# Kernel tuning notes

Hardware: AMD Instinct MI355X
Metric: run time of the kernel (lower is better)

Reference implementation:

```python
import jax, jax.numpy as jnp
import numpy as np

B, S, D = 2, 4096, 1024
H, DK = 16, 64          # heads, QK feature dim per head
DV = D // H             # output features per head = 64
QKV_OUT = (2 * DK + DV) * H  # 3072


def setup_inputs() -> dict:
    key = jax.random.key(0)
    k1, k2, k3, k4, k5 = jax.random.split(key, 5)
    x = jax.random.normal(k1, (B, S, D), dtype=jnp.float32)
    Wqkv = jax.random.normal(k2, (D, QKV_OUT), dtype=jnp.float32) * (1.0 / np.sqrt(D))
    bqkv = jnp.zeros((QKV_OUT,), dtype=jnp.float32)
    Wproj = jax.random.normal(k3, (D, D), dtype=jnp.float32) * (1.0 / np.sqrt(D))
    bproj = jnp.zeros((D,), dtype=jnp.float32)
    return {"x": x, "Wqkv": Wqkv, "bqkv": bqkv, "Wproj": Wproj, "bproj": bproj}


def reference(x, Wqkv, bqkv, Wproj, bproj):
    # QKV projection: [B,S,(2*DK+DV)*H]
    qkv = x @ Wqkv + bqkv
    q_len = DK * H
    Q = qkv[:, :, :q_len].reshape(B, S, H, DK).transpose(0, 2, 1, 3)        # [B,H,S,DK]
    K = qkv[:, :, q_len:2 * q_len].reshape(B, S, H, DK).transpose(0, 2, 1, 3)
    V = qkv[:, :, 2 * q_len:].reshape(B, S, H, DV).transpose(0, 2, 1, 3)    # [B,H,S,DV]

    scores = jnp.einsum("bhqd,bhkd->bhqk", Q, K) * (1.0 / np.sqrt(DK))
    # Faithful to source: causal mask is tril(ones) with zeros -> -inf,
    # i.e. +1.0 is ADDED on allowed positions (harmless constant shift per row).
    tril = jnp.tril(jnp.ones((S, S), dtype=jnp.float32))
    mask = jnp.where(tril == 0, -jnp.inf, tril)
    scores = scores + mask
    attn = jax.nn.softmax(scores, axis=-1)  # dropout disabled (p=0 / eval)

    out = jnp.einsum("bhqk,bhkd->bhqd", attn, V)            # [B,H,S,DV]
    out = out.transpose(0, 2, 1, 3).reshape(B, S, H * DV)   # [B,S,D]
    return out @ Wproj + bproj
```

## Files before the change

kernel.cpp:

```cpp
#include <hip/hip_runtime.h>
#include <stdint.h>


typedef __bf16 bf16x8 __attribute__((ext_vector_type(8)));
typedef float f32x4 __attribute__((ext_vector_type(4)));
typedef unsigned short u16x8 __attribute__((ext_vector_type(8)));
typedef unsigned short u16x4 __attribute__((ext_vector_type(4)));
typedef unsigned int u32x4 __attribute__((ext_vector_type(4)));

__device__ __forceinline__ unsigned short f2bf(float f) {
  unsigned u = __builtin_bit_cast(unsigned, f);
  u += 0x7FFFu + ((u >> 16) & 1u);
  return (unsigned short)(u >> 16);
}

__device__ __forceinline__ float fast_exp2(float x) {
#if __has_builtin(__builtin_amdgcn_exp2f)
  return __builtin_amdgcn_exp2f(x);
#else
  return exp2f(x);
#endif
}

__device__ __forceinline__ void gload16(const void* g, void* l) {
  __builtin_amdgcn_global_load_lds(
      (__attribute__((address_space(1))) unsigned int*)(uintptr_t)g,
      (__attribute__((address_space(3))) unsigned int*)(unsigned int)(uintptr_t)l,
      16, 0, 0);
}

__global__ void k_cvt_bf16(const float* __restrict__ in,
                           unsigned short* __restrict__ out, int n8) {
  int i = blockIdx.x * blockDim.x + threadIdx.x;
  if (i >= n8) return;
  const float4* p = reinterpret_cast<const float4*>(in) + (size_t)i * 2;
  float4 a = p[0], b = p[1];
  u16x8 o;
  o[0] = f2bf(a.x); o[1] = f2bf(a.y); o[2] = f2bf(a.z); o[3] = f2bf(a.w);
  o[4] = f2bf(b.x); o[5] = f2bf(b.y); o[6] = f2bf(b.z); o[7] = f2bf(b.w);
  *(reinterpret_cast<u16x8*>(out) + i) = o;
}

__global__ void k_transcvt(const float* __restrict__ in,
                           unsigned short* __restrict__ out, int K, int N) {
  __shared__ float tile[32][33];
  int tk0 = blockIdx.y << 5, tn0 = blockIdx.x << 5;
  int t = threadIdx.x;
  int r = t >> 3, c4 = (t & 7) << 2;
  float4 v = *reinterpret_cast<const float4*>(&in[(size_t)(tk0 + r) * N + tn0 + c4]);
  tile[r][c4 + 0] = v.x; tile[r][c4 + 1] = v.y;
  tile[r][c4 + 2] = v.z; tile[r][c4 + 3] = v.w;
  __syncthreads();
  u16x4 o;
  o[0] = f2bf(tile[c4 + 0][r]); o[1] = f2bf(tile[c4 + 1][r]);
  o[2] = f2bf(tile[c4 + 2][r]); o[3] = f2bf(tile[c4 + 3][r]);
  *reinterpret_cast<u16x4*>(&out[(size_t)(tn0 + r) * K + tk0 + c4]) = o;
}

__device__ __forceinline__ void gemm_core_db(
    const unsigned short* __restrict__ A, const unsigned short* __restrict__ Bt,
    unsigned short (*Al)[128 * 32], unsigned short (*Bl)[128 * 32],
    int m0, int n0, f32x4 acc[4][4]) {
  const int t = threadIdx.x;
  const int lane = t & 63;
  const int w = t >> 6;
  const int wr = w >> 1, wc = w & 1;
  const int l15 = lane & 15, l4 = lane >> 4;

  const int c0 = t, c1 = t + 256;
  const int r0 = c0 >> 2, s0 = ((c0 & 3) << 3) ^ (((r0 >> 1) & 3) << 3);
  const int r1 = c1 >> 2, s1 = ((c1 & 3) << 3) ^ (((r1 >> 1) & 3) << 3);
  const size_t ga0 = (size_t)(m0 + r0) * 1024 + s0;
  const size_t ga1 = (size_t)(m0 + r1) * 1024 + s1;
  const size_t gb0 = (size_t)(n0 + r0) * 1024 + s0;
  const size_t gb1 = (size_t)(n0 + r1) * 1024 + s1;

  int aidx[4], bidx[4];
#pragma unroll
  for (int m = 0; m < 4; ++m) {
    int row = wr * 64 + m * 16 + l15;
    aidx[m] = row * 32 + ((l4 * 8) ^ (((row >> 1) & 3) << 3));
    row = wc * 64 + m * 16 + l15;
    bidx[m] = row * 32 + ((l4 * 8) ^ (((row >> 1) & 3) << 3));
  }

#define GSTAGE(bufi, kofs)                                   \
  do {                                                       \
    gload16(A + ga0 + (kofs), Al[bufi] + c0 * 8);            \
    gload16(A + ga1 + (kofs), Al[bufi] + c1 * 8);            \
    gload16(Bt + gb0 + (kofs), Bl[bufi] + c0 * 8);           \
    gload16(Bt + gb1 + (kofs), Bl[bufi] + c1 * 8);           \
  } while (0)

  GSTAGE(0, 0);
  asm volatile("s_waitcnt vmcnt(0)" ::: "memory");
  __builtin_amdgcn_s_barrier();

#pragma unroll 1
  for (int it = 0; it < 32; ++it) {
    const int cur = it & 1;
    if (it + 1 < 32) GSTAGE(cur ^ 1, (it + 1) * 32);
    bf16x8 af[4], bfr[4];
#pragma unroll
    for (int m = 0; m < 4; ++m)
      af[m] = *reinterpret_cast<const bf16x8*>(Al[cur] + aidx[m]);
#pragma unroll
    for (int n = 0; n < 4; ++n)
      bfr[n] = *reinterpret_cast<const bf16x8*>(Bl[cur] + bidx[n]);
    __builtin_amdgcn_s_setprio(1);
#pragma unroll
    for (int m = 0; m < 4; ++m)
#pragma unroll
      for (int n = 0; n < 4; ++n)
        acc[m][n] = __builtin_amdgcn_mfma_f32_16x16x32_bf16(af[m], bfr[n],
                                                            acc[m][n], 0, 0, 0);
    __builtin_amdgcn_s_setprio(0);
    asm volatile("s_waitcnt vmcnt(0)" ::: "memory");
    __builtin_amdgcn_s_barrier();
  }
#undef GSTAGE
}

__global__ __launch_bounds__(256) void k_gemm_qkv(
    const unsigned short* __restrict__ A, const unsigned short* __restrict__ Bt,
    const float* __restrict__ bias, unsigned short* __restrict__ Qb,
    unsigned short* __restrict__ Kb, unsigned short* __restrict__ VTb) {
  __shared__ unsigned short Al[2][128 * 32];
  __shared__ unsigned short Bl[2][128 * 32];
  const int lane = threadIdx.x & 63, w = threadIdx.x >> 6;
  const int wr = w >> 1, wc = w & 1;
  const int l15 = lane & 15, l4 = lane >> 4;
  const int m0 = blockIdx.y << 7, n0 = blockIdx.x << 7;
  const float C1 = 0.18033688011112043f;

  f32x4 acc[4][4] = {};
  gemm_core_db(A, Bt, Al, Bl, m0, n0, acc);

#pragma unroll
  for (int m = 0; m < 4; ++m) {
#pragma unroll
    for (int n = 0; n < 4; ++n) {
#pragma unroll
      for (int j = 0; j < 4; ++j) {
        int row = m0 + wr * 64 + m * 16 + l4 * 4 + j;
        int col = n0 + wc * 64 + n * 16 + l15;
        float v = acc[m][n][j] + bias[col];
        int b = row >> 12, s = row & 4095;
        if (col < 1024) {
          int hh = col >> 6, d = col & 63;
          Qb[((size_t)(b * 16 + hh) * 4096 + s) * 64 + d] = f2bf(v * C1);
        } else if (col < 2048) {
          int cc = col - 1024; int hh = cc >> 6, d = cc & 63;
          Kb[((size_t)(b * 16 + hh) * 4096 + s) * 64 + d] = f2bf(v);
        } else {
          int cc = col - 2048; int hh = cc >> 6, d = cc & 63;
          VTb[((size_t)(b * 16 + hh) * 64 + d) * 4096 + s] = f2bf(v);
        }
      }
    }
  }
}

__global__ __launch_bounds__(256) void k_gemm_proj(
    const unsigned short* __restrict__ A, const unsigned short* __restrict__ Bt,
    const float* __restrict__ bias, float* __restrict__ out) {
  __shared__ unsigned short Al[2][128 * 32];
  __shared__ unsigned short Bl[2][128 * 32];
  const int lane = threadIdx.x & 63, w = threadIdx.x >> 6;
  const int wr = w >> 1, wc = w & 1;
  const int l15 = lane & 15, l4 = lane >> 4;
  const int m0 = blockIdx.y << 7, n0 = blockIdx.x << 7;

  f32x4 acc[4][4] = {};
  gemm_core_db(A, Bt, Al, Bl, m0, n0, acc);

#pragma unroll
  for (int m = 0; m < 4; ++m) {
#pragma unroll
    for (int n = 0; n < 4; ++n) {
#pragma unroll
      for (int j = 0; j < 4; ++j) {
        int row = m0 + wr * 64 + m * 16 + l4 * 4 + j;
        int col = n0 + wc * 64 + n * 16 + l15;
        out[(size_t)row * 1024 + col] = acc[m][n][j] + bias[col];
      }
    }
  }
}

__global__ __launch_bounds__(256, 4) void k_attn(
    const unsigned short* __restrict__ Qb, const unsigned short* __restrict__ Kb,
    const unsigned short* __restrict__ VTb, unsigned short* __restrict__ Ob) {
  __shared__ unsigned short Kl[2][64 * 64];
  __shared__ unsigned short Vl[2][64 * 64];
  const int t = threadIdx.x;
  const int lane = t & 63, w = t >> 6;
  const int l15 = lane & 15, l4 = lane >> 4;
  const int idx = blockIdx.x;
  const int qt = 31 - (idx >> 5);
  const int bh = idx & 31;
  const size_t qkbase = (size_t)bh * 4096 * 64;
  const size_t vbase = (size_t)bh * 64 * 4096;
  const int b = bh >> 4, hh = bh & 15;
  const int wrow0 = qt * 128 + w * 32;
  const int nt = 2 * qt + 2;

  const int c0 = t, c1 = t + 256;
  const int kr0 = c0 >> 3, ks0 = ((c0 & 7) << 3) ^ ((kr0 & 7) << 3);
  const int kr1 = c1 >> 3, ks1 = ((c1 & 7) << 3) ^ ((kr1 & 7) << 3);

#define STAGE(bufi, jt)                                                             \
  do {                                                                              \
    gload16(Kb + qkbase + (size_t)((jt) * 64 + kr0) * 64 + ks0, &Kl[bufi][c0 * 8]); \
    gload16(Kb + qkbase + (size_t)((jt) * 64 + kr1) * 64 + ks1, &Kl[bufi][c1 * 8]); \
    gload16(VTb + vbase + (size_t)kr0 * 4096 + (jt) * 64 + ks0, &Vl[bufi][c0 * 8]); \
    gload16(VTb + vbase + (size_t)kr1 * 4096 + (jt) * 64 + ks1, &Vl[bufi][c1 * 8]); \
  } while (0)

  bf16x8 qf[2][2];
#pragma unroll
  for (int m = 0; m < 2; ++m)
#pragma unroll
    for (int kk = 0; kk < 2; ++kk)
      qf[m][kk] = *reinterpret_cast<const bf16x8*>(
          &Qb[qkbase + (size_t)(wrow0 + m * 16 + l15) * 64 + kk * 32 + l4 * 8]);

  f32x4 oacc[2][4] = {};
  float lsum[2] = {};

  STAGE(0, 0);
  asm volatile("s_waitcnt vmcnt(0)" ::: "memory");
  __builtin_amdgcn_s_barrier();

  for (int j = 0; j < nt; ++j) {
    const int cur = j & 1;
    if (j + 1 < nt) STAGE(cur ^ 1, j + 1);

    const int jk0 = j * 64;
    const bool active = (jk0 <= wrow0 + 31);
    const bool needmask = active && (jk0 + 63 > wrow0);

    if (active) {
#pragma unroll
      for (int h = 0; h < 2; ++h) {
        f32x4 sch[2][2] = {};
        __builtin_amdgcn_s_setprio(1);
#pragma unroll
        for (int nn = 0; nn < 2; ++nn) {
          int krow = (h * 2 + nn) * 16 + l15;
#pragma unroll
          for (int kk = 0; kk < 2; ++kk) {
            int kcol = (kk * 32 + l4 * 8) ^ ((krow & 7) << 3);
            bf16x8 kfr = *reinterpret_cast<const bf16x8*>(&Kl[cur][krow * 64 + kcol]);
#pragma unroll
            for (int m = 0; m < 2; ++m)
              sch[m][nn] = __builtin_amdgcn_mfma_f32_16x16x32_bf16(
                  kfr, qf[m][kk], sch[m][nn], 0, 0, 0);
          }
        }
        __builtin_amdgcn_s_setprio(0);

        bf16x8 pa[2];
#pragma unroll
        for (int m = 0; m < 2; ++m) {
#pragma unroll
          for (int nn = 0; nn < 2; ++nn)
#pragma unroll
            for (int r = 0; r < 4; ++r)
              sch[m][nn][r] = fast_exp2(sch[m][nn][r]);
          if (needmask) {
            const int qg = wrow0 + m * 16 + l15;
#pragma unroll
            for (int nn = 0; nn < 2; ++nn) {
              const int kb = jk0 + (h * 2 + nn) * 16 + l4 * 4;
#pragma unroll
              for (int r = 0; r < 4; ++r)
                if (kb + r > qg) sch[m][nn][r] = 0.f;
            }
          }
#pragma unroll
          for (int nn = 0; nn < 2; ++nn)
#pragma unroll
            for (int r = 0; r < 4; ++r)
              lsum[m] += sch[m][nn][r];

          unsigned A0, A1, B0, B1;
          asm("v_cvt_pk_bf16_f32 %0, %1, %2"
              : "=v"(A0) : "v"(sch[m][0][0]), "v"(sch[m][0][1]));
          asm("v_cvt_pk_bf16_f32 %0, %1, %2"
              : "=v"(A1) : "v"(sch[m][0][2]), "v"(sch[m][0][3]));
          asm("v_cvt_pk_bf16_f32 %0, %1, %2"
              : "=v"(B0) : "v"(sch[m][1][0]), "v"(sch[m][1][1]));
          asm("v_cvt_pk_bf16_f32 %0, %1, %2"
              : "=v"(B1) : "v"(sch[m][1][2]), "v"(sch[m][1][3]));
          asm("v_permlane32_swap_b32 %0, %1" : "+v"(A0), "+v"(B0));
          asm("v_permlane16_swap_b32 %0, %1" : "+v"(A0), "+v"(B0));
          asm("v_permlane32_swap_b32 %0, %1" : "+v"(A1), "+v"(B1));
          asm("v_permlane16_swap_b32 %0, %1" : "+v"(A1), "+v"(B1));
          u32x4 pw;
          pw[0] = A0; pw[1] = A1; pw[2] = B0; pw[3] = B1;
          pa[m] = __builtin_bit_cast(bf16x8, pw);
        }

        __builtin_amdgcn_s_setprio(1);
#pragma unroll
        for (int nn2 = 0; nn2 < 4; ++nn2) {
          int vr = nn2 * 16 + l15;
          int vc = (h * 32 + l4 * 8) ^ ((vr & 7) << 3);
          bf16x8 vf = *reinterpret_cast<const bf16x8*>(&Vl[cur][vr * 64 + vc]);
          oacc[0][nn2] = __builtin_amdgcn_mfma_f32_16x16x32_bf16(
              pa[0], vf, oacc[0][nn2], 0, 0, 0);
          oacc[1][nn2] = __builtin_amdgcn_mfma_f32_16x16x32_bf16(
              pa[1], vf, oacc[1][nn2], 0, 0, 0);
        }
        __builtin_amdgcn_s_setprio(0);
      }
    }

    asm volatile("s_waitcnt vmcnt(0)" ::: "memory");
    __builtin_amdgcn_s_barrier();
  }
#undef STAGE

#pragma unroll
  for (int m = 0; m < 2; ++m) {
    lsum[m] += __shfl_xor(lsum[m], 16);
    lsum[m] += __shfl_xor(lsum[m], 32);
  }
#pragma unroll
  for (int m = 0; m < 2; ++m)
#pragma unroll
    for (int jj = 0; jj < 4; ++jj) {
      float inv = 1.0f / __shfl(lsum[m], l4 * 4 + jj);
      int srow = wrow0 + m * 16 + l4 * 4 + jj;
#pragma unroll
      for (int nn = 0; nn < 4; ++nn) {
        int col = hh * 64 + nn * 16 + l15;
        Ob[((size_t)(b * 4096 + srow)) * 1024 + col] =
            __builtin_bit_cast(unsigned short, (__bf16)(oacc[m][nn][jj] * inv));
      }
    }
}

extern "C" void kernel_launch(void* const* d_in, const int* in_sizes, int n_in,
                              void* d_out, int out_size, void* d_ws, size_t ws_size,
                              hipStream_t stream) {
  const float* x = (const float*)d_in[0];
  const float* Wqkv = (const float*)d_in[1];
  const float* bqkv = (const float*)d_in[2];
  const float* Wproj = (const float*)d_in[3];
  const float* bproj = (const float*)d_in[4];

  char* ws = (char*)d_ws;
  unsigned short* xb  = (unsigned short*)(ws);
  unsigned short* Wqb = (unsigned short*)(ws + 16777216);
  unsigned short* Wpb = (unsigned short*)(ws + 23068672);
  unsigned short* Qb  = (unsigned short*)(ws + 25165824);
  unsigned short* Kb  = (unsigned short*)(ws + 41943040);
  unsigned short* VTb = (unsigned short*)(ws + 58720256);
  unsigned short* Ob  = (unsigned short*)(ws + 75497472);

  k_cvt_bf16<<<dim3(8388608 / 8 / 256), dim3(256), 0, stream>>>(x, xb, 8388608 / 8);
  k_transcvt<<<dim3(3072 / 32, 1024 / 32), dim3(256), 0, stream>>>(Wqkv, Wqb, 1024, 3072);
  k_transcvt<<<dim3(1024 / 32, 1024 / 32), dim3(256), 0, stream>>>(Wproj, Wpb, 1024, 1024);
  k_gemm_qkv<<<dim3(3072 / 128, 8192 / 128), dim3(256), 0, stream>>>(xb, Wqb, bqkv, Qb, Kb, VTb);
  k_attn<<<dim3(1024), dim3(256), 0, stream>>>(Qb, Kb, VTb, Ob);
  k_gemm_proj<<<dim3(1024 / 128, 8192 / 128), dim3(256), 0, stream>>>(Ob, Wpb, bproj, (float*)d_out);
}
```

Baseline: 220.4 us.

## Load GEMM B operand straight from global into registers, unroll double buffer

The shared GEMM core now stages only the A tile through LDS. The B fragments are read directly from global memory into registers, double-buffered across a two-step unrolled loop, which removes the B LDS writes and reads and halves LDS use. The QKV epilogue hoists the bias loads, splits the Q/K and V paths by block column, and writes V-transpose as packed 4-element stores. Occupancy hints of 3 blocks are added. In exchange, global B loads are less coalesced and each wave reloads B from L2, and register pressure rises.

```diff
diff --git a/kernel.cpp b/kernel.cpp
--- a/kernel.cpp
+++ b/kernel.cpp
@@ -57,10 +57,9 @@
   *reinterpret_cast<u16x4*>(&out[(size_t)(tn0 + r) * K + tk0 + c4]) = o;
 }
 
-__device__ __forceinline__ void gemm_core_db(
+__device__ __forceinline__ void gemm_core_bg(
     const unsigned short* __restrict__ A, const unsigned short* __restrict__ Bt,
-    unsigned short (*Al)[128 * 32], unsigned short (*Bl)[128 * 32],
-    int m0, int n0, f32x4 acc[4][4]) {
+    unsigned short (*Al)[128 * 32], int m0, int n0, f32x4 acc[4][4]) {
   const int t = threadIdx.x;
   const int lane = t & 63;
   const int w = t >> 6;
@@ -72,61 +71,73 @@
   const int r1 = c1 >> 2, s1 = ((c1 & 3) << 3) ^ (((r1 >> 1) & 3) << 3);
   const size_t ga0 = (size_t)(m0 + r0) * 1024 + s0;
   const size_t ga1 = (size_t)(m0 + r1) * 1024 + s1;
-  const size_t gb0 = (size_t)(n0 + r0) * 1024 + s0;
-  const size_t gb1 = (size_t)(n0 + r1) * 1024 + s1;
-
-  int aidx[4], bidx[4];
+
+  int aidx[4];
 #pragma unroll
   for (int m = 0; m < 4; ++m) {
     int row = wr * 64 + m * 16 + l15;
     aidx[m] = row * 32 + ((l4 * 8) ^ (((row >> 1) & 3) << 3));
-    row = wc * 64 + m * 16 + l15;
-    bidx[m] = row * 32 + ((l4 * 8) ^ (((row >> 1) & 3) << 3));
-  }
-
-#define GSTAGE(bufi, kofs)                                   \
+  }
+
+  const unsigned short* bp[4];
+#pragma unroll
+  for (int n = 0; n < 4; ++n)
+    bp[n] = Bt + (size_t)(n0 + wc * 64 + n * 16 + l15) * 1024 + l4 * 8;
+
+#define ASTAGE(bufi, kofs)                                   \
   do {                                                       \
     gload16(A + ga0 + (kofs), Al[bufi] + c0 * 8);            \
     gload16(A + ga1 + (kofs), Al[bufi] + c1 * 8);            \
-    gload16(Bt + gb0 + (kofs), Bl[bufi] + c0 * 8);           \
-    gload16(Bt + gb1 + (kofs), Bl[bufi] + c1 * 8);           \
   } while (0)
 
-  GSTAGE(0, 0);
+#define BLOAD(dst, kofs)                                                     \
+  do {                                                                       \
+    _Pragma("unroll") for (int n = 0; n < 4; ++n)                            \
+      dst[n] = *reinterpret_cast<const bf16x8*>(bp[n] + (kofs));             \
+  } while (0)
+
+#define BODY(bufi, breg)                                                     \
+  do {                                                                       \
+    bf16x8 af[4];                                                            \
+    _Pragma("unroll") for (int m = 0; m < 4; ++m)                            \
+      af[m] = *reinterpret_cast<const bf16x8*>(Al[bufi] + aidx[m]);          \
+    __builtin_amdgcn_s_setprio(1);                                           \
+    _Pragma("unroll") for (int m = 0; m < 4; ++m)                            \
+      _Pragma("unroll") for (int n = 0; n < 4; ++n)                          \
+        acc[m][n] = __builtin_amdgcn_mfma_f32_16x16x32_bf16(af[m], breg[n],  \
+                                                            acc[m][n], 0, 0, 0); \
+    __builtin_amdgcn_s_setprio(0);                                           \
+    asm volatile("s_waitcnt vmcnt(0)" ::: "memory");                         \
+    __builtin_amdgcn_s_barrier();                                            \
+  } while (0)
+
+  bf16x8 b0[4], b1[4];
+  ASTAGE(0, 0);
+  BLOAD(b0, 0);
   asm volatile("s_waitcnt vmcnt(0)" ::: "memory");
   __builtin_amdgcn_s_barrier();
 
 #pragma unroll 1
-  for (int it = 0; it < 32; ++it) {
-    const int cur = it & 1;
-    if (it + 1 < 32) GSTAGE(cur ^ 1, (it + 1) * 32);
-    bf16x8 af[4], bfr[4];
-#pragma unroll
-    for (int m = 0; m < 4; ++m)
-      af[m] = *reinterpret_cast<const bf16x8*>(Al[cur] + aidx[m]);
-#pragma unroll
-    for (int n = 0; n < 4; ++n)
-      bfr[n] = *reinterpret_cast<const bf16x8*>(Bl[cur] + bidx[n]);
-    __builtin_amdgcn_s_setprio(1);
-#pragma unroll
-    for (int m = 0; m < 4; ++m)
-#pragma unroll
-      for (int n = 0; n < 4; ++n)
-        acc[m][n] = __builtin_amdgcn_mfma_f32_16x16x32_bf16(af[m], bfr[n],
-                                                            acc[m][n], 0, 0, 0);
-    __builtin_amdgcn_s_setprio(0);
-    asm volatile("s_waitcnt vmcnt(0)" ::: "memory");
-    __builtin_amdgcn_s_barrier();
-  }
-#undef GSTAGE
-}
-
-__global__ __launch_bounds__(256) void k_gemm_qkv(
+  for (int it = 0; it < 32; it += 2) {
+    ASTAGE(1, (it + 1) * 32);
+    BLOAD(b1, (it + 1) * 32);
+    BODY(0, b0);
+    if (it + 2 < 32) {
+      ASTAGE(0, (it + 2) * 32);
+      BLOAD(b0, (it + 2) * 32);
+    }
+    BODY(1, b1);
+  }
+#undef ASTAGE
+#undef BLOAD
+#undef BODY
+}
+
+__global__ __launch_bounds__(256, 3) void k_gemm_qkv(
     const unsigned short* __restrict__ A, const unsigned short* __restrict__ Bt,
     const float* __restrict__ bias, unsigned short* __restrict__ Qb,
     unsigned short* __restrict__ Kb, unsigned short* __restrict__ VTb) {
   __shared__ unsigned short Al[2][128 * 32];
-  __shared__ unsigned short Bl[2][128 * 32];
   const int lane = threadIdx.x & 63, w = threadIdx.x >> 6;
   const int wr = w >> 1, wc = w & 1;
   const int l15 = lane & 15, l4 = lane >> 4;
@@ -134,45 +145,60 @@
   const float C1 = 0.18033688011112043f;
 
   f32x4 acc[4][4] = {};
-  gemm_core_db(A, Bt, Al, Bl, m0, n0, acc);
-
-#pragma unroll
-  for (int m = 0; m < 4; ++m) {
-#pragma unroll
-    for (int n = 0; n < 4; ++n) {
-#pragma unroll
-      for (int j = 0; j < 4; ++j) {
-        int row = m0 + wr * 64 + m * 16 + l4 * 4 + j;
-        int col = n0 + wc * 64 + n * 16 + l15;
-        float v = acc[m][n][j] + bias[col];
-        int b = row >> 12, s = row & 4095;
-        if (col < 1024) {
-          int hh = col >> 6, d = col & 63;
-          Qb[((size_t)(b * 16 + hh) * 4096 + s) * 64 + d] = f2bf(v * C1);
-        } else if (col < 2048) {
-          int cc = col - 1024; int hh = cc >> 6, d = cc & 63;
-          Kb[((size_t)(b * 16 + hh) * 4096 + s) * 64 + d] = f2bf(v);
-        } else {
-          int cc = col - 2048; int hh = cc >> 6, d = cc & 63;
-          VTb[((size_t)(b * 16 + hh) * 64 + d) * 4096 + s] = f2bf(v);
+  gemm_core_bg(A, Bt, Al, m0, n0, acc);
+
+  float bi[4];
+#pragma unroll
+  for (int n = 0; n < 4; ++n) bi[n] = bias[n0 + wc * 64 + n * 16 + l15];
+
+  if (n0 < 2048) {
+#pragma unroll
+    for (int m = 0; m < 4; ++m)
+#pragma unroll
+      for (int n = 0; n < 4; ++n)
+#pragma unroll
+        for (int j = 0; j < 4; ++j) {
+          int row = m0 + wr * 64 + m * 16 + l4 * 4 + j;
+          int col = n0 + wc * 64 + n * 16 + l15;
+          float v = acc[m][n][j] + bi[n];
+          int b = row >> 12, s = row & 4095;
+          if (col < 1024) {
+            int hh = col >> 6, d = col & 63;
+            Qb[((size_t)(b * 16 + hh) * 4096 + s) * 64 + d] = f2bf(v * C1);
+          } else {
+            int cc = col - 1024; int hh = cc >> 6, d = cc & 63;
+            Kb[((size_t)(b * 16 + hh) * 4096 + s) * 64 + d] = f2bf(v);
+          }
         }
+  } else {
+#pragma unroll
+    for (int m = 0; m < 4; ++m)
+#pragma unroll
+      for (int n = 0; n < 4; ++n) {
+        int row0 = m0 + wr * 64 + m * 16 + l4 * 4;
+        int cc = n0 - 2048 + wc * 64 + n * 16 + l15;
+        int b = row0 >> 12, s0 = row0 & 4095;
+        int hh = cc >> 6, d = cc & 63;
+        u16x4 pk;
+#pragma unroll
+        for (int j = 0; j < 4; ++j) pk[j] = f2bf(acc[m][n][j] + bi[n]);
+        *reinterpret_cast<u16x4*>(
+            &VTb[((size_t)(b * 16 + hh) * 64 + d) * 4096 + s0]) = pk;
       }
-    }
-  }
-}
-
-__global__ __launch_bounds__(256) void k_gemm_proj(
+  }
+}
+
+__global__ __launch_bounds__(256, 3) void k_gemm_proj(
     const unsigned short* __restrict__ A, const unsigned short* __restrict__ Bt,
     const float* __restrict__ bias, float* __restrict__ out) {
   __shared__ unsigned short Al[2][128 * 32];
-  __shared__ unsigned short Bl[2][128 * 32];
   const int lane = threadIdx.x & 63, w = threadIdx.x >> 6;
   const int wr = w >> 1, wc = w & 1;
   const int l15 = lane & 15, l4 = lane >> 4;
   const int m0 = blockIdx.y << 7, n0 = blockIdx.x << 7;
 
   f32x4 acc[4][4] = {};
-  gemm_core_db(A, Bt, Al, Bl, m0, n0, acc);
+  gemm_core_bg(A, Bt, Al, m0, n0, acc);
 
 #pragma unroll
   for (int m = 0; m < 4; ++m) {
```

Measured after the change: 257.4 us. 16.8% more time.

## Vectorize V-transpose epilogue stores and rebalance causal attention tile ordering

Applied to the files above, without the earlier changes.

The QKV GEMM epilogue now hoists the bias loads and splits the work by column block. The V-transposed output is written as packed 4-element bf16 vectors along the sequence dimension, replacing scattered 2-byte stores. The attention kernel's query-tile ordering is changed to a zigzag schedule across four rounds of 256 blocks, so heavy and light causal tiles are interleaved in each wave for better load balance. Loop variables were renamed to avoid clashing with the new round variable.

```diff
diff --git a/kernel.cpp b/kernel.cpp
--- a/kernel.cpp
+++ b/kernel.cpp
@@ -136,28 +136,44 @@
   f32x4 acc[4][4] = {};
   gemm_core_db(A, Bt, Al, Bl, m0, n0, acc);
 
-#pragma unroll
-  for (int m = 0; m < 4; ++m) {
-#pragma unroll
-    for (int n = 0; n < 4; ++n) {
-#pragma unroll
-      for (int j = 0; j < 4; ++j) {
-        int row = m0 + wr * 64 + m * 16 + l4 * 4 + j;
-        int col = n0 + wc * 64 + n * 16 + l15;
-        float v = acc[m][n][j] + bias[col];
-        int b = row >> 12, s = row & 4095;
-        if (col < 1024) {
-          int hh = col >> 6, d = col & 63;
-          Qb[((size_t)(b * 16 + hh) * 4096 + s) * 64 + d] = f2bf(v * C1);
-        } else if (col < 2048) {
-          int cc = col - 1024; int hh = cc >> 6, d = cc & 63;
-          Kb[((size_t)(b * 16 + hh) * 4096 + s) * 64 + d] = f2bf(v);
-        } else {
-          int cc = col - 2048; int hh = cc >> 6, d = cc & 63;
-          VTb[((size_t)(b * 16 + hh) * 64 + d) * 4096 + s] = f2bf(v);
+  float bi[4];
+#pragma unroll
+  for (int n = 0; n < 4; ++n) bi[n] = bias[n0 + wc * 64 + n * 16 + l15];
+
+  if (n0 < 2048) {
+#pragma unroll
+    for (int m = 0; m < 4; ++m)
+#pragma unroll
+      for (int n = 0; n < 4; ++n)
+#pragma unroll
+        for (int j = 0; j < 4; ++j) {
+          int row = m0 + wr * 64 + m * 16 + l4 * 4 + j;
+          int col = n0 + wc * 64 + n * 16 + l15;
+          float v = acc[m][n][j] + bi[n];
+          int b = row >> 12, s = row & 4095;
+          if (col < 1024) {
+            int hh = col >> 6, d = col & 63;
+            Qb[((size_t)(b * 16 + hh) * 4096 + s) * 64 + d] = f2bf(v * C1);
+          } else {
+            int cc = col - 1024; int hh = cc >> 6, d = cc & 63;
+            Kb[((size_t)(b * 16 + hh) * 4096 + s) * 64 + d] = f2bf(v);
+          }
         }
+  } else {
+#pragma unroll
+    for (int m = 0; m < 4; ++m)
+#pragma unroll
+      for (int n = 0; n < 4; ++n) {
+        int row0 = m0 + wr * 64 + m * 16 + l4 * 4;
+        int cc = n0 - 2048 + wc * 64 + n * 16 + l15;
+        int b = row0 >> 12, s0 = row0 & 4095;
+        int hh = cc >> 6, d = cc & 63;
+        u16x4 pk;
+#pragma unroll
+        for (int j = 0; j < 4; ++j) pk[j] = f2bf(acc[m][n][j] + bi[n]);
+        *reinterpret_cast<u16x4*>(
+            &VTb[((size_t)(b * 16 + hh) * 64 + d) * 4096 + s0]) = pk;
       }
-    }
   }
 }
 
@@ -197,8 +213,11 @@
   const int lane = t & 63, w = t >> 6;
   const int l15 = lane & 15, l4 = lane >> 4;
   const int idx = blockIdx.x;
-  const int qt = 31 - (idx >> 5);
+  const int r = idx >> 8;
+  const int g = (idx >> 5) & 7;
   const int bh = idx & 31;
+  const int qt = (r == 0) ? (31 - g) : (r == 1) ? (16 + g)
+               : (r == 2) ? (15 - g) : g;
   const size_t qkbase = (size_t)bh * 4096 * 64;
   const size_t vbase = (size_t)bh * 64 * 4096;
   const int b = bh >> 4, hh = bh & 15;
@@ -266,23 +285,23 @@
 #pragma unroll
           for (int nn = 0; nn < 2; ++nn)
 #pragma unroll
-            for (int r = 0; r < 4; ++r)
-              sch[m][nn][r] = fast_exp2(sch[m][nn][r]);
+            for (int r2 = 0; r2 < 4; ++r2)
+              sch[m][nn][r2] = fast_exp2(sch[m][nn][r2]);
           if (needmask) {
             const int qg = wrow0 + m * 16 + l15;
 #pragma unroll
             for (int nn = 0; nn < 2; ++nn) {
               const int kb = jk0 + (h * 2 + nn) * 16 + l4 * 4;
 #pragma unroll
-              for (int r = 0; r < 4; ++r)
-                if (kb + r > qg) sch[m][nn][r] = 0.f;
+              for (int r2 = 0; r2 < 4; ++r2)
+                if (kb + r2 > qg) sch[m][nn][r2] = 0.f;
             }
           }
 #pragma unroll
           for (int nn = 0; nn < 2; ++nn)
 #pragma unroll
-            for (int r = 0; r < 4; ++r)
-              lsum[m] += sch[m][nn][r];
+            for (int r2 = 0; r2 < 4; ++r2)
+              lsum[m] += sch[m][nn][r2];
 
           unsigned A0, A1, B0, B1;
           asm("v_cvt_pk_bf16_f32 %0, %1, %2"
```

Result: faster. 199.5 us (-9.5%).
